# Optimization experiments

Hardware: AMD Instinct MI355X
Metric: run time of the kernel (lower is better)

Reference implementation:

```python
import jax, jax.numpy as jnp
import numpy as np

B, LD, LP, DIM = 8, 128, 1000, 128
LN_EPS = 1e-5


def layer_norm(x, gamma, beta, eps=LN_EPS):
    mu = jnp.mean(x, axis=-1, keepdims=True)
    var = jnp.mean(jnp.square(x - mu), axis=-1, keepdims=True)
    return (x - mu) * jax.lax.rsqrt(var + eps) * gamma + beta


def setup_inputs() -> dict:
    key = jax.random.key(0)
    ks = jax.random.split(key, 8)
    s = 1.0 / np.sqrt(DIM)
    return {
        "drug_conv": jax.random.normal(ks[0], (B, LD, DIM), dtype=jnp.float32),
        "protein_conv": jax.random.normal(ks[1], (B, LP, DIM), dtype=jnp.float32),
        "W_d": jax.random.normal(ks[2], (DIM, DIM), dtype=jnp.float32) * s,
        "b_d": jnp.zeros((DIM,), dtype=jnp.float32),
        "W_p": jax.random.normal(ks[3], (DIM, DIM), dtype=jnp.float32) * s,
        "b_p": jnp.zeros((DIM,), dtype=jnp.float32),
        "W_att": jax.random.normal(ks[4], (DIM, DIM), dtype=jnp.float32) * s,
        "b_att": jnp.zeros((DIM,), dtype=jnp.float32),
        "gamma1": jnp.ones((DIM,), dtype=jnp.float32),
        "beta1": jnp.zeros((DIM,), dtype=jnp.float32),
        "gamma2": jnp.ones((DIM,), dtype=jnp.float32),
        "beta2": jnp.zeros((DIM,), dtype=jnp.float32),
    }


def reference(drug_conv, protein_conv, W_d, b_d, W_p, b_p, W_att, b_att,
              gamma1, beta1, gamma2, beta2):
    # drug_conv: (B, LD, DIM), protein_conv: (B, LP, DIM)
    d_att = drug_conv @ W_d.T + b_d        # (B, LD, DIM)
    p_att = protein_conv @ W_p.T + b_p     # (B, LP, DIM)
    # Pairwise additive interaction (B, LD, LP, DIM) -- the fusable hotspot.
    M = jax.nn.relu(d_att[:, :, None, :] + p_att[:, None, :, :])
    # Linear commutes with mean: apply attention_layer after reduction.
    compound_att = jax.nn.sigmoid(jnp.mean(M, axis=2) @ W_att.T + b_att)  # (B, LD, DIM)
    protein_att = jax.nn.sigmoid(jnp.mean(M, axis=1) @ W_att.T + b_att)   # (B, LP, DIM)
    drug = drug_conv * 0.5 + drug_conv * compound_att
    prot = protein_conv * 0.5 + protein_conv * protein_att
    # MaxPool1d over full length axis == max over L, then LayerNorm(dim).
    drug_vec = layer_norm(jnp.max(drug, axis=1), gamma1, beta1)   # (B, DIM)
    prot_vec = layer_norm(jnp.max(prot, axis=1), gamma2, beta2)   # (B, DIM)
    return (drug_vec, prot_vec)
```

## Files before the change

kernel.cpp:

```cpp
#include <hip/hip_runtime.h>
#include <math.h>

#define B 8
#define LD 128
#define LP 1000
#define LP_PAD 1008
#define DIM 128
#define LN_EPS 1e-5f

#define TILES_D (B * LD / 16)
#define TILES_P (B * LP / 16)
#define GTILES_D 64
#define GTILES_PB 63
#define GTILES_P (8 * GTILES_PB)
#define SEG_D 8
#define SEG_P GTILES_PB

typedef __attribute__((ext_vector_type(8))) short bf16x8;
typedef __attribute__((ext_vector_type(4))) float f32x4;

__device__ inline short f2bf(float f) {
    union { float f; unsigned u; } v; v.f = f;
    unsigned r = v.u + 0x7fffu + ((v.u >> 16) & 1u);
    return (short)(r >> 16);
}

__device__ inline bf16x8 cvt8(float4 lo, float4 hi) {
    bf16x8 r;
    r[0] = f2bf(lo.x); r[1] = f2bf(lo.y); r[2] = f2bf(lo.z); r[3] = f2bf(lo.w);
    r[4] = f2bf(hi.x); r[5] = f2bf(hi.y); r[6] = f2bf(hi.z); r[7] = f2bf(hi.w);
    return r;
}

__global__ __launch_bounds__(256) void conv_w(const float* __restrict__ W0,
                                              const float* __restrict__ W1,
                                              const float* __restrict__ W2,
                                              short* __restrict__ out) {
    const int idx = blockIdx.x * 256 + threadIdx.x;
    const float* src = idx < 16384 ? W0 : (idx < 32768 ? W1 : W2);
    out[idx] = f2bf(src[idx & 16383]);
}

__global__ __launch_bounds__(256) void mfma_gemv(
        const float* __restrict__ Xd, const float* __restrict__ Xp,
        const short* __restrict__ Wdb, const float* __restrict__ bd,
        const short* __restrict__ Wpb, const float* __restrict__ bp,
        float* __restrict__ outd, float* __restrict__ outp) {
    const int wave = (blockIdx.x * 256 + threadIdx.x) >> 6;
    const int lane = threadIdx.x & 63;

    const float* X; const short* Wb; const float* bias; float* out; int m0;
    if (wave < TILES_D) { X = Xd; Wb = Wdb; bias = bd; out = outd; m0 = wave * 16; }
    else { X = Xp; Wb = Wpb; bias = bp; out = outp; m0 = (wave - TILES_D) * 16; }

    const int arow = lane & 15;
    const int kgrp = lane >> 4;

    bf16x8 afrag[4];
    {
        const float* xrow = X + (size_t)(m0 + arow) * DIM + kgrp * 8;
#pragma unroll
        for (int kk = 0; kk < 4; ++kk)
            afrag[kk] = cvt8(*(const float4*)(xrow + kk * 32),
                             *(const float4*)(xrow + kk * 32 + 4));
    }

    const int ocol = lane & 15;
    const int orow = (lane >> 4) * 4;
#pragma unroll
    for (int nt = 0; nt < 8; ++nt) {
        const short* wrow = Wb + (size_t)(nt * 16 + arow) * DIM + kgrp * 8;
        f32x4 c = {0.f, 0.f, 0.f, 0.f};
#pragma unroll
        for (int kk = 0; kk < 4; ++kk) {
            const bf16x8 bfrag = *(const bf16x8*)(wrow + kk * 32);
            c = __builtin_amdgcn_mfma_f32_16x16x32_bf16(afrag[kk], bfrag, c, 0, 0, 0);
        }
        const float bv = bias[nt * 16 + ocol];
#pragma unroll
        for (int r = 0; r < 4; ++r)
            out[(size_t)(m0 + orow + r) * DIM + nt * 16 + ocol] = c[r] + bv;
    }
}

__global__ __launch_bounds__(256) void pairwise(
        const float* __restrict__ d_att, const float* __restrict__ p_att,
        float* __restrict__ Mc, float* __restrict__ Mp) {
    const int blk = blockIdx.x;
    const int b = blk >> 7;
    const int d = blk & (DIM - 1);
    const int t = threadIdx.x;

    __shared__ float xs[LD];
    __shared__ float2 ys2[LP_PAD / 2];
    __shared__ float red[LD * 8];

    if (t < LD) xs[t] = d_att[(b * LD + t) * DIM + d];
    for (int j = t; j < LP_PAD; j += 256) {
        ((float*)ys2)[j] = (j < LP) ? p_att[(b * LP + j) * DIM + d] : -1e30f;
    }
    __syncthreads();

    for (int p = t; p < LP_PAD / 2; p += 256) {
        const float2 y = ys2[p];
        float2 acc = make_float2(0.f, 0.f);
#pragma unroll 8
        for (int i = 0; i < LD; ++i) {
            const float x = xs[i];
            acc.x += fmaxf(0.f, x + y.x);
            acc.y += fmaxf(0.f, x + y.y);
        }
        const int j = 2 * p;
        if (j < LP)     Mp[(b * LP + j) * DIM + d]     = acc.x * (1.f / (float)LD);
        if (j + 1 < LP) Mp[(b * LP + j + 1) * DIM + d] = acc.y * (1.f / (float)LD);
    }

    {
        const int rq = t >> 3;
        const int sl = t & 7;
        const float x0 = xs[4 * rq + 0];
        const float x1 = xs[4 * rq + 1];
        const float x2 = xs[4 * rq + 2];
        const float x3 = xs[4 * rq + 3];
        float2 a0 = make_float2(0.f, 0.f), a1 = a0, a2 = a0, a3 = a0;
        for (int p = sl; p < LP_PAD / 2; p += 8) {
            const float2 y = ys2[p];
            a0.x += fmaxf(0.f, x0 + y.x); a0.y += fmaxf(0.f, x0 + y.y);
            a1.x += fmaxf(0.f, x1 + y.x); a1.y += fmaxf(0.f, x1 + y.y);
            a2.x += fmaxf(0.f, x2 + y.x); a2.y += fmaxf(0.f, x2 + y.y);
            a3.x += fmaxf(0.f, x3 + y.x); a3.y += fmaxf(0.f, x3 + y.y);
        }
        red[(4 * rq + 0) * 8 + sl] = a0.x + a0.y;
        red[(4 * rq + 1) * 8 + sl] = a1.x + a1.y;
        red[(4 * rq + 2) * 8 + sl] = a2.x + a2.y;
        red[(4 * rq + 3) * 8 + sl] = a3.x + a3.y;
    }
    __syncthreads();
    if (t < LD) {
        float s = 0.f;
#pragma unroll
        for (int k = 0; k < 8; ++k) s += red[t * 8 + k];
        Mc[(b * LD + t) * DIM + d] = s * (1.f / (float)LP);
    }
}

__global__ __launch_bounds__(256) void mfma_gated(
        const float* __restrict__ Mc, const float* __restrict__ Mp,
        const short* __restrict__ Wb, const float* __restrict__ bias,
        const float* __restrict__ convd, const float* __restrict__ convp,
        float* __restrict__ pd, float* __restrict__ pp) {
    const int wave = (blockIdx.x * 256 + threadIdx.x) >> 6;
    const int lane = threadIdx.x & 63;

    const float* M; const float* conv; float* part; int m0; int valid;
    if (wave < GTILES_D) {
        M = Mc; conv = convd; part = pd + wave * DIM; m0 = wave * 16; valid = 16;
    } else {
        const int pb = wave - GTILES_D;
        const int b = pb / GTILES_PB;
        const int s = pb - b * GTILES_PB;
        M = Mp; conv = convp; part = pp + pb * DIM;
        m0 = b * LP + s * 16;
        valid = (s * 16 + 16 <= LP) ? 16 : (LP - s * 16);
    }

    const int arow = lane & 15;
    const int kgrp = lane >> 4;

    bf16x8 afrag[4];
    if (arow < valid) {
        const float* mrow = M + (size_t)(m0 + arow) * DIM + kgrp * 8;
#pragma unroll
        for (int kk = 0; kk < 4; ++kk)
            afrag[kk] = cvt8(*(const float4*)(mrow + kk * 32),
                             *(const float4*)(mrow + kk * 32 + 4));
    } else {
        bf16x8 z;
#pragma unroll
        for (int j = 0; j < 8; ++j) z[j] = 0;
#pragma unroll
        for (int kk = 0; kk < 4; ++kk) afrag[kk] = z;
    }

    const int ocol = lane & 15;
    const int orow = (lane >> 4) * 4;
#pragma unroll
    for (int nt = 0; nt < 8; ++nt) {
        const short* wrow = Wb + (size_t)(nt * 16 + arow) * DIM + kgrp * 8;
        f32x4 c = {0.f, 0.f, 0.f, 0.f};
#pragma unroll
        for (int kk = 0; kk < 4; ++kk) {
            const bf16x8 bfrag = *(const bf16x8*)(wrow + kk * 32);
            c = __builtin_amdgcn_mfma_f32_16x16x32_bf16(afrag[kk], bfrag, c, 0, 0, 0);
        }
        const float bv = bias[nt * 16 + ocol];
        float m = -INFINITY;
#pragma unroll
        for (int r = 0; r < 4; ++r) {
            const int rr = orow + r;
            if (rr < valid) {
                const float att = 1.f / (1.f + __expf(-(c[r] + bv)));
                const float v = conv[(size_t)(m0 + rr) * DIM + nt * 16 + ocol] * (0.5f + att);
                m = fmaxf(m, v);
            }
        }
        m = fmaxf(m, __shfl_xor(m, 16));
        m = fmaxf(m, __shfl_xor(m, 32));
        if (lane < 16) part[nt * 16 + lane] = m;
    }
}

__global__ __launch_bounds__(256) void maxln_final(
        const float* __restrict__ pd, const float* __restrict__ pp,
        const float* __restrict__ gamma1, const float* __restrict__ beta1,
        const float* __restrict__ gamma2, const float* __restrict__ beta2,
        float* __restrict__ out) {
    const int blk = blockIdx.x;
    const int kind = blk >> 3;
    const int b = blk & 7;
    const int t = threadIdx.x & (DIM - 1);
    const int h = threadIdx.x >> 7;

    float m = -INFINITY;
    if (kind == 0) {
        const float* base = pd + b * SEG_D * DIM;
        for (int s = h; s < SEG_D; s += 2) m = fmaxf(m, base[s * DIM + t]);
    } else {
        const float* base = pp + b * SEG_P * DIM;
        for (int s = h; s < SEG_P; s += 2) m = fmaxf(m, base[s * DIM + t]);
    }

    __shared__ float sm[2][DIM];
    sm[h][t] = m;
    __syncthreads();

    __shared__ float s1[DIM];
    __shared__ float s2[DIM];
    if (threadIdx.x < DIM) {
        m = fmaxf(sm[0][t], sm[1][t]);
        sm[0][t] = m;
        s1[t] = m;
        s2[t] = m * m;
    }
    __syncthreads();
    for (int off = DIM / 2; off > 0; off >>= 1) {
        if (threadIdx.x < off) {
            s1[threadIdx.x] += s1[threadIdx.x + off];
            s2[threadIdx.x] += s2[threadIdx.x + off];
        }
        __syncthreads();
    }
    if (threadIdx.x < DIM) {
        const float mu = s1[0] * (1.f / (float)DIM);
        const float var = s2[0] * (1.f / (float)DIM) - mu * mu;
        const float inv = rsqrtf(var + LN_EPS);
        const float* gamma = kind ? gamma2 : gamma1;
        const float* beta  = kind ? beta2  : beta1;
        out[blk * DIM + t] = (sm[0][t] - mu) * inv * gamma[t] + beta[t];
    }
}

extern "C" void kernel_launch(void* const* d_in, const int* in_sizes, int n_in,
                              void* d_out, int out_size, void* d_ws, size_t ws_size,
                              hipStream_t stream) {
    const float* drug_conv    = (const float*)d_in[0];
    const float* protein_conv = (const float*)d_in[1];
    const float* W_d   = (const float*)d_in[2];
    const float* b_d   = (const float*)d_in[3];
    const float* W_p   = (const float*)d_in[4];
    const float* b_p   = (const float*)d_in[5];
    const float* W_att = (const float*)d_in[6];
    const float* b_att = (const float*)d_in[7];
    const float* gamma1 = (const float*)d_in[8];
    const float* beta1  = (const float*)d_in[9];
    const float* gamma2 = (const float*)d_in[10];
    const float* beta2  = (const float*)d_in[11];
    float* out = (float*)d_out;

    float* ws = (float*)d_ws;
    const size_t n_datt = (size_t)B * LD * DIM;
    const size_t n_patt = (size_t)B * LP * DIM;
    float* d_att = ws;
    float* p_att = ws + n_datt;
    float* Mc    = ws + n_datt + n_patt;
    float* Mp    = ws + n_datt + n_patt + n_datt;
    short* wbf   = (short*)(ws + 2310144);
    short* wb_d   = wbf;
    short* wb_p   = wbf + 16384;
    short* wb_att = wbf + 32768;
    float* pd = ws;
    float* pp = ws + GTILES_D * DIM;

    conv_w<<<192, 256, 0, stream>>>(W_d, W_p, W_att, wbf);
    mfma_gemv<<<(TILES_D + TILES_P) / 4, 256, 0, stream>>>(
        drug_conv, protein_conv, wb_d, b_d, wb_p, b_p, d_att, p_att);
    pairwise<<<B * DIM, 256, 0, stream>>>(d_att, p_att, Mc, Mp);
    mfma_gated<<<(GTILES_D + GTILES_P) / 4, 256, 0, stream>>>(
        Mc, Mp, wb_att, b_att, drug_conv, protein_conv, pd, pp);
    maxln_final<<<16, 256, 0, stream>>>(pd, pp, gamma1, beta1, gamma2, beta2, out);
}
```

Before: 140.2 us.

## Drop weight-conversion kernel, convert weights inline, widen pairwise LDS reads

Removes the separate conv_w launch and instead converts the fp32 weights to bf16 inside each MFMA kernel as they are loaded, using the HIP bf16 intrinsic for rounding. The protein buffer is padded to 1024 entries so each pairwise thread handles exactly two float2 column pairs with no loop, and the compound-reduction loop reads float4 from LDS. This saves one kernel launch and the weight round-trip through memory, but every wave now reads fp32 weights and converts them again. The wider LDS reads and fixed work split cut loop and load overhead in the hot pairwise kernel.

```diff
diff --git a/kernel.cpp b/kernel.cpp
--- a/kernel.cpp
+++ b/kernel.cpp
@@ -1,10 +1,11 @@
 #include <hip/hip_runtime.h>
+#include <hip/hip_bf16.h>
 #include <math.h>
 
 #define B 8
 #define LD 128
 #define LP 1000
-#define LP_PAD 1008
+#define LP_PAD 1024
 #define DIM 128
 #define LN_EPS 1e-5f
 
@@ -20,9 +21,7 @@
 typedef __attribute__((ext_vector_type(4))) float f32x4;
 
 __device__ inline short f2bf(float f) {
-    union { float f; unsigned u; } v; v.f = f;
-    unsigned r = v.u + 0x7fffu + ((v.u >> 16) & 1u);
-    return (short)(r >> 16);
+    return __bfloat16_as_short(__float2bfloat16(f));
 }
 
 __device__ inline bf16x8 cvt8(float4 lo, float4 hi) {
@@ -32,26 +31,17 @@
     return r;
 }
 
-__global__ __launch_bounds__(256) void conv_w(const float* __restrict__ W0,
-                                              const float* __restrict__ W1,
-                                              const float* __restrict__ W2,
-                                              short* __restrict__ out) {
-    const int idx = blockIdx.x * 256 + threadIdx.x;
-    const float* src = idx < 16384 ? W0 : (idx < 32768 ? W1 : W2);
-    out[idx] = f2bf(src[idx & 16383]);
-}
-
 __global__ __launch_bounds__(256) void mfma_gemv(
         const float* __restrict__ Xd, const float* __restrict__ Xp,
-        const short* __restrict__ Wdb, const float* __restrict__ bd,
-        const short* __restrict__ Wpb, const float* __restrict__ bp,
+        const float* __restrict__ Wd, const float* __restrict__ bd,
+        const float* __restrict__ Wp, const float* __restrict__ bp,
         float* __restrict__ outd, float* __restrict__ outp) {
     const int wave = (blockIdx.x * 256 + threadIdx.x) >> 6;
     const int lane = threadIdx.x & 63;
 
-    const float* X; const short* Wb; const float* bias; float* out; int m0;
-    if (wave < TILES_D) { X = Xd; Wb = Wdb; bias = bd; out = outd; m0 = wave * 16; }
-    else { X = Xp; Wb = Wpb; bias = bp; out = outp; m0 = (wave - TILES_D) * 16; }
+    const float* X; const float* W; const float* bias; float* out; int m0;
+    if (wave < TILES_D) { X = Xd; W = Wd; bias = bd; out = outd; m0 = wave * 16; }
+    else { X = Xp; W = Wp; bias = bp; out = outp; m0 = (wave - TILES_D) * 16; }
 
     const int arow = lane & 15;
     const int kgrp = lane >> 4;
@@ -69,11 +59,12 @@
     const int orow = (lane >> 4) * 4;
 #pragma unroll
     for (int nt = 0; nt < 8; ++nt) {
-        const short* wrow = Wb + (size_t)(nt * 16 + arow) * DIM + kgrp * 8;
+        const float* wrow = W + (size_t)(nt * 16 + arow) * DIM + kgrp * 8;
         f32x4 c = {0.f, 0.f, 0.f, 0.f};
 #pragma unroll
         for (int kk = 0; kk < 4; ++kk) {
-            const bf16x8 bfrag = *(const bf16x8*)(wrow + kk * 32);
+            const bf16x8 bfrag = cvt8(*(const float4*)(wrow + kk * 32),
+                                      *(const float4*)(wrow + kk * 32 + 4));
             c = __builtin_amdgcn_mfma_f32_16x16x32_bf16(afrag[kk], bfrag, c, 0, 0, 0);
         }
         const float bv = bias[nt * 16 + ocol];
@@ -92,27 +83,36 @@
     const int t = threadIdx.x;
 
     __shared__ float xs[LD];
-    __shared__ float2 ys2[LP_PAD / 2];
+    __shared__ float ys[LP_PAD];
     __shared__ float red[LD * 8];
 
     if (t < LD) xs[t] = d_att[(b * LD + t) * DIM + d];
     for (int j = t; j < LP_PAD; j += 256) {
-        ((float*)ys2)[j] = (j < LP) ? p_att[(b * LP + j) * DIM + d] : -1e30f;
+        ys[j] = (j < LP) ? p_att[(b * LP + j) * DIM + d] : -1e30f;
     }
     __syncthreads();
 
-    for (int p = t; p < LP_PAD / 2; p += 256) {
-        const float2 y = ys2[p];
-        float2 acc = make_float2(0.f, 0.f);
+    const float2* ys2 = (const float2*)ys;
+    const float4* ys4 = (const float4*)ys;
+
+    {
+        const float2 y0 = ys2[t];
+        const float2 y1 = ys2[t + 256];
+        float2 acc0 = make_float2(0.f, 0.f), acc1 = acc0;
 #pragma unroll 8
         for (int i = 0; i < LD; ++i) {
             const float x = xs[i];
-            acc.x += fmaxf(0.f, x + y.x);
-            acc.y += fmaxf(0.f, x + y.y);
-        }
-        const int j = 2 * p;
-        if (j < LP)     Mp[(b * LP + j) * DIM + d]     = acc.x * (1.f / (float)LD);
-        if (j + 1 < LP) Mp[(b * LP + j + 1) * DIM + d] = acc.y * (1.f / (float)LD);
+            acc0.x += fmaxf(0.f, x + y0.x);
+            acc0.y += fmaxf(0.f, x + y0.y);
+            acc1.x += fmaxf(0.f, x + y1.x);
+            acc1.y += fmaxf(0.f, x + y1.y);
+        }
+        const int j0 = 2 * t;
+        Mp[(b * LP + j0) * DIM + d]     = acc0.x * (1.f / (float)LD);
+        Mp[(b * LP + j0 + 1) * DIM + d] = acc0.y * (1.f / (float)LD);
+        const int j1 = 512 + 2 * t;
+        if (j1 < LP)     Mp[(b * LP + j1) * DIM + d]     = acc1.x * (1.f / (float)LD);
+        if (j1 + 1 < LP) Mp[(b * LP + j1 + 1) * DIM + d] = acc1.y * (1.f / (float)LD);
     }
 
     {
@@ -123,12 +123,16 @@
         const float x2 = xs[4 * rq + 2];
         const float x3 = xs[4 * rq + 3];
         float2 a0 = make_float2(0.f, 0.f), a1 = a0, a2 = a0, a3 = a0;
-        for (int p = sl; p < LP_PAD / 2; p += 8) {
-            const float2 y = ys2[p];
+        for (int q = sl; q < LP_PAD / 4; q += 8) {
+            const float4 y = ys4[q];
             a0.x += fmaxf(0.f, x0 + y.x); a0.y += fmaxf(0.f, x0 + y.y);
+            a0.x += fmaxf(0.f, x0 + y.z); a0.y += fmaxf(0.f, x0 + y.w);
             a1.x += fmaxf(0.f, x1 + y.x); a1.y += fmaxf(0.f, x1 + y.y);
+            a1.x += fmaxf(0.f, x1 + y.z); a1.y += fmaxf(0.f, x1 + y.w);
             a2.x += fmaxf(0.f, x2 + y.x); a2.y += fmaxf(0.f, x2 + y.y);
+            a2.x += fmaxf(0.f, x2 + y.z); a2.y += fmaxf(0.f, x2 + y.w);
             a3.x += fmaxf(0.f, x3 + y.x); a3.y += fmaxf(0.f, x3 + y.y);
+            a3.x += fmaxf(0.f, x3 + y.z); a3.y += fmaxf(0.f, x3 + y.w);
         }
         red[(4 * rq + 0) * 8 + sl] = a0.x + a0.y;
         red[(4 * rq + 1) * 8 + sl] = a1.x + a1.y;
@@ -146,7 +150,7 @@
 
 __global__ __launch_bounds__(256) void mfma_gated(
         const float* __restrict__ Mc, const float* __restrict__ Mp,
-        const short* __restrict__ Wb, const float* __restrict__ bias,
+        const float* __restrict__ W, const float* __restrict__ bias,
         const float* __restrict__ convd, const float* __restrict__ convp,
         float* __restrict__ pd, float* __restrict__ pp) {
     const int wave = (blockIdx.x * 256 + threadIdx.x) >> 6;
@@ -186,11 +190,12 @@
     const int orow = (lane >> 4) * 4;
 #pragma unroll
     for (int nt = 0; nt < 8; ++nt) {
-        const short* wrow = Wb + (size_t)(nt * 16 + arow) * DIM + kgrp * 8;
+        const float* wrow = W + (size_t)(nt * 16 + arow) * DIM + kgrp * 8;
         f32x4 c = {0.f, 0.f, 0.f, 0.f};
 #pragma unroll
         for (int kk = 0; kk < 4; ++kk) {
-            const bf16x8 bfrag = *(const bf16x8*)(wrow + kk * 32);
+            const bf16x8 bfrag = cvt8(*(const float4*)(wrow + kk * 32),
+                                      *(const float4*)(wrow + kk * 32 + 4));
             c = __builtin_amdgcn_mfma_f32_16x16x32_bf16(afrag[kk], bfrag, c, 0, 0, 0);
         }
         const float bv = bias[nt * 16 + ocol];
@@ -284,18 +289,13 @@
     float* p_att = ws + n_datt;
     float* Mc    = ws + n_datt + n_patt;
     float* Mp    = ws + n_datt + n_patt + n_datt;
-    short* wbf   = (short*)(ws + 2310144);
-    short* wb_d   = wbf;
-    short* wb_p   = wbf + 16384;
-    short* wb_att = wbf + 32768;
     float* pd = ws;
     float* pp = ws + GTILES_D * DIM;
 
-    conv_w<<<192, 256, 0, stream>>>(W_d, W_p, W_att, wbf);
     mfma_gemv<<<(TILES_D + TILES_P) / 4, 256, 0, stream>>>(
-        drug_conv, protein_conv, wb_d, b_d, wb_p, b_p, d_att, p_att);
+        drug_conv, protein_conv, W_d, b_d, W_p, b_p, d_att, p_att);
     pairwise<<<B * DIM, 256, 0, stream>>>(d_att, p_att, Mc, Mp);
     mfma_gated<<<(GTILES_D + GTILES_P) / 4, 256, 0, stream>>>(
-        Mc, Mp, wb_att, b_att, drug_conv, protein_conv, pd, pp);
+        Mc, Mp, W_att, b_att, drug_conv, protein_conv, pd, pp);
     maxln_final<<<16, 256, 0, stream>>>(pd, pp, gamma1, beta1, gamma2, beta2, out);
 }
```

After: 141.2 us. About the same (+0.7%).
